# Kernel tuning notes

Measured on AMD Instinct MI355X. Metric: run time of the kernel, lower is better.

The kernel has to match this reference:

```python
import jax, jax.numpy as jnp
import numpy as np

V, D, L, H, S, B = 32000, 512, 4, 8, 2048, 2
HD = D // H
FF = 4 * D
EPS = 1e-5


def _ln(x, w, b):
    m = jnp.mean(x, axis=-1, keepdims=True)
    v = jnp.var(x, axis=-1, keepdims=True)
    return (x - m) / jnp.sqrt(v + EPS) * w + b


def setup_inputs() -> dict:
    key = jax.random.key(0)
    ks = jax.random.split(key, 32)
    rn = lambda k, shape, s=0.02: jax.random.normal(k, shape, jnp.float32) * s
    return {
        'x': jax.random.randint(ks[0], (B, S), 0, V),
        'tok_emb': rn(ks[1], (V, D)),
        'pos_emb': rn(ks[2], (S, D)),
        'qw': rn(ks[3], (L, D, D)), 'qb': rn(ks[4], (L, D)),
        'kw': rn(ks[5], (L, D, D)), 'kb': rn(ks[6], (L, D)),
        'vw': rn(ks[7], (L, D, D)), 'vb': rn(ks[8], (L, D)),
        'ow': rn(ks[9], (L, D, D)), 'ob': rn(ks[10], (L, D)),
        'qphase': rn(ks[11], (L, H), 0.1),
        'sp_phase': rn(ks[12], (L, D), 0.1),
        'n1w': jnp.ones((L, D), jnp.float32), 'n1b': jnp.zeros((L, D), jnp.float32),
        'n2w': jnp.ones((L, D), jnp.float32), 'n2b': jnp.zeros((L, D), jnp.float32),
        'f1w': rn(ks[13], (L, D, FF)), 'f1b': rn(ks[14], (L, FF)),
        'f2w': rn(ks[15], (L, FF, D)), 'f2b': rn(ks[16], (L, D)),
        'iw': rn(ks[17], (L, D, D)), 'ib': rn(ks[18], (L, D)),
        'gw': rn(ks[19], (L, D, D)), 'gb': rn(ks[20], (L, D)),
        'nw': jnp.ones((D,), jnp.float32), 'nb': jnp.zeros((D,), jnp.float32),
        'outw': rn(ks[21], (D, V)), 'outb': rn(ks[22], (V,)),
    }


def _forward(x, tok_emb, pos_emb, qw, qb, kw, kb, vw, vb, ow, ob, qphase, sp_phase,
             n1w, n1b, n2w, n2b, f1w, f1b, f2w, f2b, iw, ib, gw, gb, nw, nb, outw, outb):
    Bx, Sx = x.shape
    h = tok_emb[x] + pos_emb[:Sx][None, :, :]          # [B,S,D]
    mask = jnp.tril(jnp.ones((Sx, Sx), dtype=bool))    # causal
    scale = 1.0 / np.sqrt(HD).astype(np.float32)
    for l in range(L):
        # quantum attention with phase-modulated scores
        hn = _ln(h, n1w[l], n1b[l])
        q = (hn @ qw[l] + qb[l]).reshape(Bx, Sx, H, HD)
        k = (hn @ kw[l] + kb[l]).reshape(Bx, Sx, H, HD)
        v = (hn @ vw[l] + vb[l]).reshape(Bx, Sx, H, HD)
        scores = jnp.einsum('bqhd,bkhd->bhqk', q, k) * scale
        qi = jnp.cos(qphase[l][None, :, None, None] * scores)
        scores = scores * (1.0 + 0.1 * qi)
        scores = jnp.where(mask[None, None], scores, -jnp.inf)
        attn = jax.nn.softmax(scores, axis=-1)
        o = jnp.einsum('bhqk,bkhd->bqhd', attn, v).reshape(Bx, Sx, D)
        h = h + o @ ow[l] + ob[l]
        # superposition: x * cos(phase * x)
        h = h * jnp.cos(sp_phase[l] * h)
        # feed-forward (exact GELU, as torch default)
        hn2 = _ln(h, n2w[l], n2b[l])
        h = h + jax.nn.gelu(hn2 @ f1w[l] + f1b[l], approximate=False) @ f2w[l] + f2b[l]
        # interference gate
        g = jax.nn.sigmoid(h @ gw[l] + gb[l])
        h = (h @ iw[l] + ib[l]) * g + h * (1.0 - g)
    h = _ln(h, nw, nb)
    return h @ outw + outb                              # [B,S,V] logits


def reference(x, tok_emb, pos_emb, qw, qb, kw, kb, vw, vb, ow, ob, qphase, sp_phase,
              n1w, n1b, n2w, n2b, f1w, f1b, f2w, f2b, iw, ib, gw, gb, nw, nb, outw, outb):
    return _forward(x, tok_emb, pos_emb, qw, qb, kw, kb, vw, vb, ow, ob, qphase, sp_phase,
                    n1w, n1b, n2w, n2b, f1w, f1b, f2w, f2b, iw, ib, gw, gb, nw, nb, outw, outb)
```

## Files before the change

kernel.cpp:

```cpp
#include <hip/hip_runtime.h>
#include <math.h>

#define DIM 512
#define NH 8
#define HD 64
#define SEQ 2048
#define BATCH 2
#define NLAYER 4
#define FFD 2048
#define VOCAB 32000
#define ROWS (BATCH*SEQ)
#define QKV_LD 1536

typedef unsigned short u16;
typedef __attribute__((ext_vector_type(8))) short bfrag;
typedef __attribute__((ext_vector_type(4))) float facc;

__device__ __forceinline__ u16 f2bf(float f){
  unsigned u = __builtin_bit_cast(unsigned, f);
  u += 0x7fff + ((u>>16)&1);
  return (u16)(u>>16);
}

typedef __attribute__((address_space(3))) unsigned int lds_u32;
typedef const __attribute__((address_space(1))) unsigned int glob_u32;
__device__ __forceinline__ void gload16(const void* g, void* l){
  __builtin_amdgcn_global_load_lds((glob_u32*)g, (lds_u32*)l, 16, 0, 0);
}

template<int N> __device__ __forceinline__ void wait_vmcnt(){
  if constexpr (N==0)      asm volatile("s_waitcnt vmcnt(0)" ::: "memory");
  else if constexpr (N==3) asm volatile("s_waitcnt vmcnt(3)" ::: "memory");
  else if constexpr (N==4) asm volatile("s_waitcnt vmcnt(4)" ::: "memory");
  else if constexpr (N==8) asm volatile("s_waitcnt vmcnt(8)" ::: "memory");
  else static_assert(N==0, "unsupported vmcnt");
}

__global__ void transpose_w(const float* __restrict__ in, u16* __restrict__ out,
                            int K, int N, size_t zStride, int nOff){
  __shared__ float t[32][33];
  const int bz = blockIdx.z;
  const float* I = in + (size_t)bz*K*N;
  u16* O = out + (size_t)bz*zStride + (size_t)nOff*K;
  const int n0 = blockIdx.x*32, k0 = blockIdx.y*32;
  #pragma unroll
  for (int i=0;i<4;i++){
    int k = k0 + threadIdx.y + 8*i;
    t[threadIdx.y+8*i][threadIdx.x] = I[(size_t)k*N + n0 + threadIdx.x];
  }
  __syncthreads();
  #pragma unroll
  for (int i=0;i<4;i++){
    int n = n0 + threadIdx.y + 8*i;
    O[(size_t)n*K + k0 + threadIdx.x] = f2bf(t[threadIdx.x][threadIdx.y+8*i]);
  }
}

__global__ void concat3_k(const float* __restrict__ a, const float* __restrict__ b,
                          const float* __restrict__ c, float* __restrict__ o){
  int idx = blockIdx.x*256 + threadIdx.x;
  int l = idx/1536, r = idx%1536;
  float v = (r<512) ? a[l*512+r] : (r<1024 ? b[l*512+r-512] : c[l*512+r-1024]);
  o[idx] = v;
}
__global__ void concat2_k(const float* __restrict__ a, const float* __restrict__ b,
                          float* __restrict__ o){
  int idx = blockIdx.x*256 + threadIdx.x;
  int l = idx>>10, r = idx&1023;
  o[idx] = (r<512) ? a[l*512+r] : b[l*512+r-512];
}

__global__ void embed_k(const int* __restrict__ x, const float* __restrict__ tok,
                        const float* __restrict__ pos, float* __restrict__ h){
  int idx = blockIdx.x*256 + threadIdx.x;
  int row = idx >> 7;
  int d4  = idx & 127;
  int s   = row & (SEQ-1);
  int tkn = x[row];
  float4 tv = *(const float4*)(tok + (size_t)tkn*DIM + d4*4);
  float4 pv = *(const float4*)(pos + (size_t)s*DIM + d4*4);
  float4 r; r.x=tv.x+pv.x; r.y=tv.y+pv.y; r.z=tv.z+pv.z; r.w=tv.w+pv.w;
  *(float4*)(h + (size_t)row*DIM + d4*4) = r;
}

__global__ __launch_bounds__(256) void ln_k(const float* __restrict__ h,
    const float* __restrict__ w, const float* __restrict__ bsc,
    u16* __restrict__ out){
  const int wid = threadIdx.x>>6, lane = threadIdx.x&63;
  const int row = blockIdx.x*4 + wid;
  const float* r = h + (size_t)row*DIM + lane*8;
  float4 v0 = *(const float4*)r;
  float4 v1 = *(const float4*)(r+4);
  float s  = v0.x+v0.y+v0.z+v0.w + v1.x+v1.y+v1.z+v1.w;
  float ss = v0.x*v0.x+v0.y*v0.y+v0.z*v0.z+v0.w*v0.w
           + v1.x*v1.x+v1.y*v1.y+v1.z*v1.z+v1.w*v1.w;
  #pragma unroll
  for (int m=1;m<64;m<<=1){ s += __shfl_xor(s,m); ss += __shfl_xor(ss,m); }
  const float mean = s*(1.f/DIM);
  const float var  = ss*(1.f/DIM) - mean*mean;
  const float rsd  = rsqrtf(var + 1e-5f);
  float4 w0 = *(const float4*)(w + lane*8);
  float4 w1 = *(const float4*)(w + lane*8 + 4);
  float4 b0 = *(const float4*)(bsc + lane*8);
  float4 b1 = *(const float4*)(bsc + lane*8 + 4);
  bfrag pk;
  pk[0]=(short)f2bf((v0.x-mean)*rsd*w0.x+b0.x);
  pk[1]=(short)f2bf((v0.y-mean)*rsd*w0.y+b0.y);
  pk[2]=(short)f2bf((v0.z-mean)*rsd*w0.z+b0.z);
  pk[3]=(short)f2bf((v0.w-mean)*rsd*w0.w+b0.w);
  pk[4]=(short)f2bf((v1.x-mean)*rsd*w1.x+b1.x);
  pk[5]=(short)f2bf((v1.y-mean)*rsd*w1.y+b1.y);
  pk[6]=(short)f2bf((v1.z-mean)*rsd*w1.z+b1.z);
  pk[7]=(short)f2bf((v1.w-mean)*rsd*w1.w+b1.w);
  *(bfrag*)&out[(size_t)row*DIM + lane*8] = pk;
}

template<int BM,int BN,int BK,int WRN,int WCN,int MODE>
__global__ __launch_bounds__(WRN*WCN*64, 2) void gemm_p(
    const u16* __restrict__ A, const u16* __restrict__ BT,
    const float* __restrict__ bias, const float* __restrict__ aux,
    float* __restrict__ Cf, u16* __restrict__ Cb,
    int M, int N, int K){
  constexpr int NTH = WRN*WCN*64;
  constexpr int FI  = BM/(16*WRN);
  constexpr int FJ  = BN/(16*WCN);
  constexpr int CPR = BK/8;
  constexpr int LA  = BM*CPR/NTH;
  constexpr int LB  = BN*CPR/NTH;
  constexpr int LPT = LA+LB;
  constexpr int NKK = BK/32;
  extern __shared__ __align__(16) u16 smem[];
  u16* lds_a = smem;
  u16* lds_b = smem + 2*BM*BK;

  const int tid = threadIdx.x;
  const int wid = tid>>6, lane = tid&63;
  const int wr = wid / WCN, wc = wid % WCN;
  const int lr = lane&15, lg = lane>>4;
  const unsigned nwg = gridDim.x*gridDim.y;
  const unsigned lin = blockIdx.y*gridDim.x + blockIdx.x;
  const unsigned q = nwg >> 3;
  const unsigned sw = (lin & 7)*q + (lin >> 3);
  const int tm = sw % gridDim.x, tn = sw / gridDim.x;

  auto swzf = [](int row)->int{ return (BK==64) ? (row&7) : ((row>>1)&3); };

  auto stage = [&](int t, int buf){
    const int k0 = t*BK;
    #pragma unroll
    for (int i=0;i<LA;i++){
      int u = i*NTH + tid;
      int row = u/CPR, c = (u%CPR) ^ swzf(row);
      gload16(&A[(size_t)(tm*BM+row)*K + k0 + c*8], &lds_a[buf*BM*BK + u*8]);
    }
    #pragma unroll
    for (int i=0;i<LB;i++){
      int u = i*NTH + tid;
      int row = u/CPR, c = (u%CPR) ^ swzf(row);
      gload16(&BT[(size_t)(tn*BN+row)*K + k0 + c*8], &lds_b[buf*BN*BK + u*8]);
    }
  };

  facc acc[FI][FJ] = {};
  const int NT = K/BK;
  stage(0,0); stage(1,1);
  for (int t=0;t<NT;t++){
    const int buf = t&1;
    const u16* la = &lds_a[buf*BM*BK];
    const u16* lb = &lds_b[buf*BN*BK];
    if (t<NT-1) wait_vmcnt<LPT>(); else wait_vmcnt<0>();
    __builtin_amdgcn_s_barrier();
    __builtin_amdgcn_sched_barrier(0);
    bfrag af[FI], bf[FJ];
    #pragma unroll
    for (int i=0;i<FI;i++){
      int row = wr*(FI*16) + i*16 + lr;
      af[i] = *(const bfrag*)&la[row*BK + ((lg ^ swzf(row))*8)];
    }
    #pragma unroll
    for (int j=0;j<FJ;j++){
      int row = wc*(FJ*16) + j*16 + lr;
      bf[j] = *(const bfrag*)&lb[row*BK + ((lg ^ swzf(row))*8)];
    }
    if constexpr (NKK==1){
      asm volatile("s_waitcnt lgkmcnt(0)" ::: "memory");
      __builtin_amdgcn_sched_barrier(0);
      __builtin_amdgcn_s_barrier();
      __builtin_amdgcn_sched_barrier(0);
      if (t+2<NT) stage(t+2, buf);
      __builtin_amdgcn_s_setprio(1);
      #pragma unroll
      for (int i=0;i<FI;i++)
        #pragma unroll
        for (int j=0;j<FJ;j++)
          acc[i][j] = __builtin_amdgcn_mfma_f32_16x16x32_bf16(af[i], bf[j], acc[i][j],0,0,0);
      __builtin_amdgcn_s_setprio(0);
    } else {
      __builtin_amdgcn_s_setprio(1);
      #pragma unroll
      for (int i=0;i<FI;i++)
        #pragma unroll
        for (int j=0;j<FJ;j++)
          acc[i][j] = __builtin_amdgcn_mfma_f32_16x16x32_bf16(af[i], bf[j], acc[i][j],0,0,0);
      __builtin_amdgcn_s_setprio(0);
      bfrag af1[FI], bf1[FJ];
      #pragma unroll
      for (int i=0;i<FI;i++){
        int row = wr*(FI*16) + i*16 + lr;
        af1[i] = *(const bfrag*)&la[row*BK + (((4+lg) ^ swzf(row))*8)];
      }
      #pragma unroll
      for (int j=0;j<FJ;j++){
        int row = wc*(FJ*16) + j*16 + lr;
        bf1[j] = *(const bfrag*)&lb[row*BK + (((4+lg) ^ swzf(row))*8)];
      }
      asm volatile("s_waitcnt lgkmcnt(0)" ::: "memory");
      __builtin_amdgcn_sched_barrier(0);
      __builtin_amdgcn_s_barrier();
      __builtin_amdgcn_sched_barrier(0);
      if (t+2<NT) stage(t+2, buf);
      __builtin_amdgcn_s_setprio(1);
      #pragma unroll
      for (int i=0;i<FI;i++)
        #pragma unroll
        for (int j=0;j<FJ;j++)
          acc[i][j] = __builtin_amdgcn_mfma_f32_16x16x32_bf16(af1[i], bf1[j], acc[i][j],0,0,0);
      __builtin_amdgcn_s_setprio(0);
    }
  }
  #pragma unroll
  for (int i=0;i<FI;i++){
    #pragma unroll
    for (int j=0;j<FJ;j++){
      const int col = tn*BN + wc*(FJ*16) + j*16 + lr;
      const float bv = bias ? bias[col] : 0.f;
      #pragma unroll
      for (int r=0;r<4;r++){
        const int row = tm*BM + wr*(FI*16) + i*16 + lg*4 + r;
        float v = acc[i][j][r] + bv;
        const size_t o = (size_t)row*N + col;
        if      (MODE==0) Cf[o] = v;
        else if (MODE==1) Cb[o] = f2bf(v);
        else if (MODE==3){ float g = 0.5f*v*(1.f+erff(v*0.70710678118f)); Cb[o] = f2bf(g); }
        else if (MODE==4){ float t = Cf[o] + v; t = t*__cosf(aux[col]*t); Cf[o] = t; }
        else if (MODE==6){ float t = Cf[o] + v; Cf[o] = t; Cb[o] = f2bf(t); }
      }
    }
  }
}

__global__ void vtrans_k(const u16* __restrict__ v, u16* __restrict__ vt){
  __shared__ u16 t[32][33];
  const int bz = blockIdx.z;
  const int b = bz / NH, hh = bz % NH;
  const int s0 = blockIdx.x*32, d0 = blockIdx.y*32;
  #pragma unroll
  for (int i=0;i<4;i++){
    int s = s0 + threadIdx.y + 8*i;
    t[threadIdx.y+8*i][threadIdx.x] = v[(size_t)(b*SEQ + s)*QKV_LD + 1024 + hh*HD + d0 + threadIdx.x];
  }
  __syncthreads();
  #pragma unroll
  for (int i=0;i<4;i++){
    int d = d0 + threadIdx.y + 8*i;
    vt[((size_t)bz*HD + d)*SEQ + s0 + threadIdx.x] = t[threadIdx.x][threadIdx.y+8*i];
  }
}

__global__ __launch_bounds__(256) void attn_k(
    const u16* __restrict__ QKV, const u16* __restrict__ VT,
    const float* __restrict__ qphase, u16* __restrict__ O){
  __shared__ __align__(16) u16 lds_p[4][16*32];
  const int qblk = blockIdx.x, hh = blockIdx.y, b = blockIdx.z;
  const int tid = threadIdx.x;
  const int wid = tid>>6, lane = tid&63;
  const int lr = lane&15, lg = lane>>4;
  const int qbase = qblk*64 + wid*16;
  const float ph = qphase[hh];
  const float scale = 0.125f;
  u16* pbuf = lds_p[wid];

  bfrag aq[2];
  #pragma unroll
  for (int st=0; st<2; st++)
    aq[st] = *(const bfrag*)&QKV[(size_t)(b*SEQ + qbase + lr)*QKV_LD + hh*HD + st*32 + lg*8];

  facc oacc[4];
  #pragma unroll
  for (int n=0;n<4;n++) oacc[n] = (facc){0.f,0.f,0.f,0.f};
  float mrow[4] = {-1e30f,-1e30f,-1e30f,-1e30f};
  float lrow[4] = {0.f,0.f,0.f,0.f};

  const int nkv = (qbase + 15)/32 + 1;
  for (int kt=0; kt<nkv; kt++){
    const int kv0 = kt*32;
    facc sc[2];
    #pragma unroll
    for (int j=0;j<2;j++){
      bfrag bk0 = *(const bfrag*)&QKV[(size_t)(b*SEQ + kv0 + j*16 + lr)*QKV_LD + 512 + hh*HD + lg*8];
      bfrag bk1 = *(const bfrag*)&QKV[(size_t)(b*SEQ + kv0 + j*16 + lr)*QKV_LD + 512 + hh*HD + 32 + lg*8];
      facc z = (facc){0.f,0.f,0.f,0.f};
      z     = __builtin_amdgcn_mfma_f32_16x16x32_bf16(aq[0], bk0, z, 0,0,0);
      sc[j] = __builtin_amdgcn_mfma_f32_16x16x32_bf16(aq[1], bk1, z, 0,0,0);
    }
    bfrag vbf[4];
    #pragma unroll
    for (int n=0;n<4;n++)
      vbf[n] = *(const bfrag*)&VT[((size_t)((b*NH + hh)*HD + n*16 + lr))*SEQ + kv0 + lg*8];

    float pv[2][4];
    float tmax[4] = {-1e30f,-1e30f,-1e30f,-1e30f};
    #pragma unroll
    for (int j=0;j<2;j++)
      #pragma unroll
      for (int r=0;r<4;r++){
        int srow = qbase + lg*4 + r;
        int scol = kv0 + j*16 + lr;
        float xv = sc[j][r]*scale;
        xv = xv*(1.f + 0.1f*__cosf(ph*xv));
        if (scol > srow) xv = -1e30f;
        pv[j][r] = xv;
        tmax[r] = fmaxf(tmax[r], xv);
      }
    #pragma unroll
    for (int r=0;r<4;r++){
      float t = tmax[r];
      t = fmaxf(t, __shfl_xor(t,1));
      t = fmaxf(t, __shfl_xor(t,2));
      t = fmaxf(t, __shfl_xor(t,4));
      t = fmaxf(t, __shfl_xor(t,8));
      float mnew = fmaxf(mrow[r], t);
      float corr = __expf(mrow[r] - mnew);
      float p0 = __expf(pv[0][r] - mnew);
      float p1 = __expf(pv[1][r] - mnew);
      pv[0][r] = p0; pv[1][r] = p1;
      float rs = p0 + p1;
      rs += __shfl_xor(rs,1);
      rs += __shfl_xor(rs,2);
      rs += __shfl_xor(rs,4);
      rs += __shfl_xor(rs,8);
      lrow[r] = lrow[r]*corr + rs;
      mrow[r] = mnew;
      #pragma unroll
      for (int n=0;n<4;n++) oacc[n][r] *= corr;
    }
    #pragma unroll
    for (int j=0;j<2;j++)
      #pragma unroll
      for (int r=0;r<4;r++)
        pbuf[(lg*4+r)*32 + j*16 + lr] = f2bf(pv[j][r]);
    bfrag pa = *(const bfrag*)&pbuf[lr*32 + lg*8];
    #pragma unroll
    for (int n=0;n<4;n++)
      oacc[n] = __builtin_amdgcn_mfma_f32_16x16x32_bf16(pa, vbf[n], oacc[n], 0,0,0);
  }
  #pragma unroll
  for (int n=0;n<4;n++)
    #pragma unroll
    for (int r=0;r<4;r++){
      float val = oacc[n][r] / lrow[r];
      O[(size_t)(b*SEQ + qbase + lg*4 + r)*DIM + hh*HD + n*16 + lr] = f2bf(val);
    }
}

__global__ void gate_k(float* __restrict__ h, const float* __restrict__ ig){
  int idx = blockIdx.x*256 + threadIdx.x;
  int row = idx >> 7, d4 = idx & 127;
  float4 hv = *(const float4*)(h  + (size_t)idx*4);
  float4 iv = *(const float4*)(ig + (size_t)row*1024 + d4*4);
  float4 gv = *(const float4*)(ig + (size_t)row*1024 + 512 + d4*4);
  float g;
  g = 1.f/(1.f+__expf(-gv.x)); hv.x = iv.x*g + hv.x*(1.f-g);
  g = 1.f/(1.f+__expf(-gv.y)); hv.y = iv.y*g + hv.y*(1.f-g);
  g = 1.f/(1.f+__expf(-gv.z)); hv.z = iv.z*g + hv.z*(1.f-g);
  g = 1.f/(1.f+__expf(-gv.w)); hv.w = iv.w*g + hv.w*(1.f-g);
  *(float4*)(h + (size_t)idx*4) = hv;
}

extern "C" void kernel_launch(void* const* d_in, const int* in_sizes, int n_in,
                              void* d_out, int out_size, void* d_ws, size_t ws_size,
                              hipStream_t stream){
  const int*   x        = (const int*)d_in[0];
  const float* tok_emb  = (const float*)d_in[1];
  const float* pos_emb  = (const float*)d_in[2];
  const float* qw = (const float*)d_in[3];  const float* qb = (const float*)d_in[4];
  const float* kw = (const float*)d_in[5];  const float* kb = (const float*)d_in[6];
  const float* vw = (const float*)d_in[7];  const float* vb = (const float*)d_in[8];
  const float* ow = (const float*)d_in[9];  const float* ob = (const float*)d_in[10];
  const float* qphase   = (const float*)d_in[11];
  const float* sp_phase = (const float*)d_in[12];
  const float* n1w = (const float*)d_in[13]; const float* n1b = (const float*)d_in[14];
  const float* n2w = (const float*)d_in[15]; const float* n2b = (const float*)d_in[16];
  const float* f1w = (const float*)d_in[17]; const float* f1b = (const float*)d_in[18];
  const float* f2w = (const float*)d_in[19]; const float* f2b = (const float*)d_in[20];
  const float* iw  = (const float*)d_in[21]; const float* ib  = (const float*)d_in[22];
  const float* gw  = (const float*)d_in[23]; const float* gb  = (const float*)d_in[24];
  const float* nw  = (const float*)d_in[25]; const float* nb  = (const float*)d_in[26];
  const float* outw= (const float*)d_in[27]; const float* outb= (const float*)d_in[28];
  float* out = (float*)d_out;

  char* base = (char*)d_ws;
  size_t off = 0;
  auto alloc = [&](size_t bytes)->void*{
    void* p = base + off; off += bytes; off = (off + 255) & ~(size_t)255; return p;
  };
  float* h    = (float*)alloc((size_t)ROWS*DIM*4);
  u16* hn     = (u16*)alloc((size_t)ROWS*DIM*2);
  u16* qkvB   = (u16*)alloc((size_t)ROWS*QKV_LD*2);
  u16* vTb    = (u16*)alloc((size_t)ROWS*DIM*2);
  u16* oB     = (u16*)alloc((size_t)ROWS*DIM*2);
  u16* hB     = (u16*)alloc((size_t)ROWS*DIM*2);
  u16* ffB    = (u16*)alloc((size_t)ROWS*FFD*2);
  float* igF  = (float*)alloc((size_t)ROWS*1024*4);
  u16* qkvT = (u16*)alloc((size_t)NLAYER*1536*DIM*2);
  u16* owT  = (u16*)alloc((size_t)NLAYER*DIM*DIM*2);
  u16* igT  = (u16*)alloc((size_t)NLAYER*1024*DIM*2);
  u16* f1T  = (u16*)alloc((size_t)NLAYER*DIM*FFD*2);
  u16* f2T  = (u16*)alloc((size_t)NLAYER*DIM*FFD*2);
  u16* outT = (u16*)alloc((size_t)VOCAB*DIM*2);
  float* qkvb = (float*)alloc((size_t)NLAYER*1536*4);
  float* igb  = (float*)alloc((size_t)NLAYER*1024*4);

  dim3 tb(32,8);
  transpose_w<<<dim3(DIM/32, DIM/32, NLAYER), tb, 0, stream>>>(qw, qkvT, DIM, DIM, (size_t)1536*DIM, 0);
  transpose_w<<<dim3(DIM/32, DIM/32, NLAYER), tb, 0, stream>>>(kw, qkvT, DIM, DIM, (size_t)1536*DIM, 512);
  transpose_w<<<dim3(DIM/32, DIM/32, NLAYER), tb, 0, stream>>>(vw, qkvT, DIM, DIM, (size_t)1536*DIM, 1024);
  transpose_w<<<dim3(DIM/32, DIM/32, NLAYER), tb, 0, stream>>>(ow, owT, DIM, DIM, (size_t)DIM*DIM, 0);
  transpose_w<<<dim3(DIM/32, DIM/32, NLAYER), tb, 0, stream>>>(iw, igT, DIM, DIM, (size_t)1024*DIM, 0);
  transpose_w<<<dim3(DIM/32, DIM/32, NLAYER), tb, 0, stream>>>(gw, igT, DIM, DIM, (size_t)1024*DIM, 512);
  transpose_w<<<dim3(FFD/32, DIM/32, NLAYER), tb, 0, stream>>>(f1w, f1T, DIM, FFD, (size_t)DIM*FFD, 0);
  transpose_w<<<dim3(DIM/32, FFD/32, NLAYER), tb, 0, stream>>>(f2w, f2T, FFD, DIM, (size_t)DIM*FFD, 0);
  transpose_w<<<dim3(VOCAB/32, DIM/32, 1),    tb, 0, stream>>>(outw, outT, DIM, VOCAB, 0, 0);
  concat3_k<<<NLAYER*1536/256, 256, 0, stream>>>(qb, kb, vb, qkvb);
  concat2_k<<<NLAYER*1024/256, 256, 0, stream>>>(ib, gb, igb);

  embed_k<<<ROWS*DIM/4/256, 256, 0, stream>>>(x, tok_emb, pos_emb, h);

  constexpr size_t SM_MID = 2*(128+128)*32*2;
  constexpr size_t SM_ROW = 2*(64+128)*32*2;
  constexpr size_t SM_BIG = 2*(256+256)*64*2;

  for (int l=0;l<NLAYER;l++){
    ln_k<<<ROWS/4, 256, 0, stream>>>(h, n1w + l*DIM, n1b + l*DIM, hn);
    gemm_p<128,128,32,2,2,1><<<dim3(ROWS/128, 1536/128), 256, SM_MID, stream>>>(
        hn, qkvT + (size_t)l*1536*DIM, qkvb + l*1536, nullptr, nullptr, qkvB, ROWS, 1536, DIM);
    vtrans_k<<<dim3(SEQ/32, HD/32, BATCH*NH), tb, 0, stream>>>(qkvB, vTb);
    attn_k<<<dim3(SEQ/64, NH, BATCH), 256, 0, stream>>>(qkvB, vTb, qphase + l*NH, oB);
    gemm_p<64,128,32,1,4,4><<<dim3(ROWS/64, DIM/128), 256, SM_ROW, stream>>>(
        oB, owT + (size_t)l*DIM*DIM, ob + l*DIM, sp_phase + l*DIM, h, nullptr, ROWS, DIM, DIM);
    ln_k<<<ROWS/4, 256, 0, stream>>>(h, n2w + l*DIM, n2b + l*DIM, hn);
    gemm_p<128,128,32,2,2,3><<<dim3(ROWS/128, FFD/128), 256, SM_MID, stream>>>(
        hn, f1T + (size_t)l*DIM*FFD, f1b + l*FFD, nullptr, nullptr, ffB, ROWS, FFD, DIM);
    gemm_p<64,128,32,1,4,6><<<dim3(ROWS/64, DIM/128), 256, SM_ROW, stream>>>(
        ffB, f2T + (size_t)l*DIM*FFD, f2b + l*DIM, nullptr, h, hB, ROWS, DIM, FFD);
    gemm_p<128,128,32,2,2,0><<<dim3(ROWS/128, 1024/128), 256, SM_MID, stream>>>(
        hB, igT + (size_t)l*1024*DIM, igb + l*1024, nullptr, igF, nullptr, ROWS, 1024, DIM);
    gate_k<<<ROWS*DIM/4/256, 256, 0, stream>>>(h, igF);
  }
  ln_k<<<ROWS/4, 256, 0, stream>>>(h, nw, nb, hn);
  gemm_p<256,256,64,2,4,0><<<dim3(ROWS/256, VOCAB/256), 512, SM_BIG, stream>>>(
      hn, outT, outb, nullptr, out, nullptr, ROWS, VOCAB, DIM);
}
```

Before: 1.209 ms.

## Drop online-softmax max tracking, widen attention KV tile, balance causal blocks

```diff
diff --git a/kernel.cpp b/kernel.cpp
--- a/kernel.cpp
+++ b/kernel.cpp
@@ -32,6 +32,7 @@
   if constexpr (N==0)      asm volatile("s_waitcnt vmcnt(0)" ::: "memory");
   else if constexpr (N==3) asm volatile("s_waitcnt vmcnt(3)" ::: "memory");
   else if constexpr (N==4) asm volatile("s_waitcnt vmcnt(4)" ::: "memory");
+  else if constexpr (N==6) asm volatile("s_waitcnt vmcnt(6)" ::: "memory");
   else if constexpr (N==8) asm volatile("s_waitcnt vmcnt(8)" ::: "memory");
   else static_assert(N==0, "unsupported vmcnt");
 }
@@ -270,8 +271,10 @@
 __global__ __launch_bounds__(256) void attn_k(
     const u16* __restrict__ QKV, const u16* __restrict__ VT,
     const float* __restrict__ qphase, u16* __restrict__ O){
-  __shared__ __align__(16) u16 lds_p[4][16*32];
-  const int qblk = blockIdx.x, hh = blockIdx.y, b = blockIdx.z;
+  __shared__ __align__(16) u16 lds_p[4][16*64];
+  const int bx = blockIdx.x;
+  const int qblk = (bx&1) ? (31 - (bx>>1)) : (bx>>1);
+  const int hh = blockIdx.y, b = blockIdx.z;
   const int tid = threadIdx.x;
   const int wid = tid>>6, lane = tid&63;
   const int lr = lane&15, lg = lane>>4;
@@ -285,33 +288,24 @@
   for (int st=0; st<2; st++)
     aq[st] = *(const bfrag*)&QKV[(size_t)(b*SEQ + qbase + lr)*QKV_LD + hh*HD + st*32 + lg*8];
 
-  facc oacc[4];
-  #pragma unroll
-  for (int n=0;n<4;n++) oacc[n] = (facc){0.f,0.f,0.f,0.f};
-  float mrow[4] = {-1e30f,-1e30f,-1e30f,-1e30f};
+  facc oacc[4] = {};
   float lrow[4] = {0.f,0.f,0.f,0.f};
 
-  const int nkv = (qbase + 15)/32 + 1;
+  const int nkv = qblk + 1;
   for (int kt=0; kt<nkv; kt++){
-    const int kv0 = kt*32;
-    facc sc[2];
-    #pragma unroll
-    for (int j=0;j<2;j++){
+    const int kv0 = kt*64;
+    facc sc[4];
+    #pragma unroll
+    for (int j=0;j<4;j++){
       bfrag bk0 = *(const bfrag*)&QKV[(size_t)(b*SEQ + kv0 + j*16 + lr)*QKV_LD + 512 + hh*HD + lg*8];
       bfrag bk1 = *(const bfrag*)&QKV[(size_t)(b*SEQ + kv0 + j*16 + lr)*QKV_LD + 512 + hh*HD + 32 + lg*8];
       facc z = (facc){0.f,0.f,0.f,0.f};
       z     = __builtin_amdgcn_mfma_f32_16x16x32_bf16(aq[0], bk0, z, 0,0,0);
       sc[j] = __builtin_amdgcn_mfma_f32_16x16x32_bf16(aq[1], bk1, z, 0,0,0);
     }
-    bfrag vbf[4];
-    #pragma unroll
-    for (int n=0;n<4;n++)
-      vbf[n] = *(const bfrag*)&VT[((size_t)((b*NH + hh)*HD + n*16 + lr))*SEQ + kv0 + lg*8];
-
-    float pv[2][4];
-    float tmax[4] = {-1e30f,-1e30f,-1e30f,-1e30f};
-    #pragma unroll
-    for (int j=0;j<2;j++)
+    float pv[4][4];
+    #pragma unroll
+    for (int j=0;j<4;j++)
       #pragma unroll
       for (int r=0;r<4;r++){
         int srow = qbase + lg*4 + r;
@@ -319,46 +313,42 @@
         float xv = sc[j][r]*scale;
         xv = xv*(1.f + 0.1f*__cosf(ph*xv));
         if (scol > srow) xv = -1e30f;
-        pv[j][r] = xv;
-        tmax[r] = fmaxf(tmax[r], xv);
+        pv[j][r] = __expf(xv);
       }
     #pragma unroll
     for (int r=0;r<4;r++){
-      float t = tmax[r];
-      t = fmaxf(t, __shfl_xor(t,1));
-      t = fmaxf(t, __shfl_xor(t,2));
-      t = fmaxf(t, __shfl_xor(t,4));
-      t = fmaxf(t, __shfl_xor(t,8));
-      float mnew = fmaxf(mrow[r], t);
-      float corr = __expf(mrow[r] - mnew);
-      float p0 = __expf(pv[0][r] - mnew);
-      float p1 = __expf(pv[1][r] - mnew);
-      pv[0][r] = p0; pv[1][r] = p1;
-      float rs = p0 + p1;
+      float rs = (pv[0][r]+pv[1][r]) + (pv[2][r]+pv[3][r]);
       rs += __shfl_xor(rs,1);
       rs += __shfl_xor(rs,2);
       rs += __shfl_xor(rs,4);
       rs += __shfl_xor(rs,8);
-      lrow[r] = lrow[r]*corr + rs;
-      mrow[r] = mnew;
-      #pragma unroll
-      for (int n=0;n<4;n++) oacc[n][r] *= corr;
-    }
-    #pragma unroll
-    for (int j=0;j<2;j++)
-      #pragma unroll
-      for (int r=0;r<4;r++)
-        pbuf[(lg*4+r)*32 + j*16 + lr] = f2bf(pv[j][r]);
-    bfrag pa = *(const bfrag*)&pbuf[lr*32 + lg*8];
-    #pragma unroll
-    for (int n=0;n<4;n++)
-      oacc[n] = __builtin_amdgcn_mfma_f32_16x16x32_bf16(pa, vbf[n], oacc[n], 0,0,0);
-  }
+      lrow[r] += rs;
+    }
+    #pragma unroll
+    for (int j=0;j<4;j++)
+      #pragma unroll
+      for (int r=0;r<4;r++){
+        int prow = lg*4 + r;
+        pbuf[prow*64 + ((j*16+lr) ^ ((prow&7)<<3))] = f2bf(pv[j][r]);
+      }
+    #pragma unroll
+    for (int ks=0; ks<2; ks++){
+      bfrag pa = *(const bfrag*)&pbuf[lr*64 + ((ks*32 + lg*8) ^ ((lr&7)<<3))];
+      #pragma unroll
+      for (int n=0;n<4;n++){
+        bfrag vb = *(const bfrag*)&VT[((size_t)((b*NH + hh)*HD + n*16 + lr))*SEQ + kv0 + ks*32 + lg*8];
+        oacc[n] = __builtin_amdgcn_mfma_f32_16x16x32_bf16(pa, vb, oacc[n], 0,0,0);
+      }
+    }
+  }
+  float rcp[4];
+  #pragma unroll
+  for (int r=0;r<4;r++) rcp[r] = 1.f/lrow[r];
   #pragma unroll
   for (int n=0;n<4;n++)
     #pragma unroll
     for (int r=0;r<4;r++){
-      float val = oacc[n][r] / lrow[r];
+      float val = oacc[n][r] * rcp[r];
       O[(size_t)(b*SEQ + qbase + lg*4 + r)*DIM + hh*HD + n*16 + lr] = f2bf(val);
     }
 }
@@ -438,7 +428,7 @@
 
   constexpr size_t SM_MID = 2*(128+128)*32*2;
   constexpr size_t SM_ROW = 2*(64+128)*32*2;
-  constexpr size_t SM_BIG = 2*(256+256)*64*2;
+  constexpr size_t SM_BIG = 2*(256+256)*32*2;
 
   for (int l=0;l<NLAYER;l++){
     ln_k<<<ROWS/4, 256, 0, stream>>>(h, n1w + l*DIM, n1b + l*DIM, hn);
@@ -458,6 +448,6 @@
     gate_k<<<ROWS*DIM/4/256, 256, 0, stream>>>(h, igF);
   }
   ln_k<<<ROWS/4, 256, 0, stream>>>(h, nw, nb, hn);
-  gemm_p<256,256,64,2,4,0><<<dim3(ROWS/256, VOCAB/256), 512, SM_BIG, stream>>>(
+  gemm_p<256,256,32,2,4,0><<<dim3(ROWS/256, VOCAB/256), 512, SM_BIG, stream>>>(
       hn, outT, outb, nullptr, out, nullptr, ROWS, VOCAB, DIM);
 }
```

Measured after the change: 1.310 ms. 1.08x slower.
